# Kernel tuning notes

Hardware: AMD Instinct MI355X
Metric: run time of the kernel (lower is better)

Reference implementation:

```python
import jax, jax.numpy as jnp
import numpy as np
import math

B, S, H, NH = 2, 2048, 1024, 16
HD = H // NH  # 64


def setup_inputs() -> dict:
    key = jax.random.key(0)
    ks = jax.random.split(key, 16)
    s = 0.02  # init scale for weights
    def lin(k, fan_in, fan_out):
        kw, kb = jax.random.split(k)
        # stored as [in, out] so y = x @ W + b (equivalent to torch Linear)
        W = jax.random.normal(kw, (fan_in, fan_out), jnp.float32) * s
        b = jax.random.normal(kb, (fan_out,), jnp.float32) * s
        return W, b
    q_w, q_b = lin(ks[2], H, H)
    k_w, k_b = lin(ks[3], H, H)
    v_w, v_b = lin(ks[4], H, H)
    o_w, o_b = lin(ks[5], H, H)
    pg_w, pg_b = lin(ks[6], 4, NH)   # prosody_gate
    mg_w, mg_b = lin(ks[7], H, 1)    # memory_gate
    return dict(
        hidden_states=jax.random.normal(ks[0], (B, S, H), jnp.float32),
        prosody=jax.random.normal(ks[1], (B, S, 4), jnp.float32),
        q_w=q_w, q_b=q_b, k_w=k_w, k_b=k_b, v_w=v_w, v_b=v_b,
        o_w=o_w, o_b=o_b, pg_w=pg_w, pg_b=pg_b, mg_w=mg_w, mg_b=mg_b,
    )


def reference(hidden_states, prosody, q_w, q_b, k_w, k_b, v_w, v_b,
              o_w, o_b, pg_w, pg_b, mg_w, mg_b):
    b, s, _ = hidden_states.shape
    # Q, K, V projections -> [B, NH, S, HD]
    def split_heads(x):
        return x.reshape(b, s, NH, HD).transpose(0, 2, 1, 3)
    q = split_heads(hidden_states @ q_w + q_b)
    k = split_heads(hidden_states @ k_w + k_b)
    v = split_heads(hidden_states @ v_w + v_b)
    # Prosody gating of queries: gain in (0,1), per (batch, head, position)
    prosody_gain = jax.nn.sigmoid(prosody @ pg_w + pg_b)      # [B, S, NH]
    prosody_gain = prosody_gain.transpose(0, 2, 1)[..., None]  # [B, NH, S, 1]
    q = q * (1.0 + prosody_gain)
    # Scaled scores [B, NH, S, S]
    scores = jnp.einsum('bhqd,bhkd->bhqk', q, k) / math.sqrt(HD)
    # Hippocampal memory scaling: per-query-position multiplicative gate
    memory_weight = jax.nn.sigmoid(hidden_states @ mg_w + mg_b)  # [B, S, 1]
    mem_scale = 1.0 + memory_weight[:, None, :, :] * 0.5         # [B, 1, S, 1]
    scores = scores * mem_scale
    # Causal mask (upper triangle above diagonal -> -inf)
    causal = jnp.tril(jnp.ones((s, s), dtype=bool))
    scores = jnp.where(causal[None, None], scores, -jnp.inf)
    attn_weights = jax.nn.softmax(scores, axis=-1)
    # (dropout is identity in eval / p=0)
    context = jnp.einsum('bhqk,bhkd->bhqd', attn_weights, v)
    context = context.transpose(0, 2, 1, 3).reshape(b, s, H)
    output = context @ o_w + o_b
    return (output, attn_weights)
```

## Files before the change

### kernel.cpp

```cpp
#include <hip/hip_runtime.h>
#include <hip/hip_bf16.h>
#include <math.h>

#define B_  2
#define S_  2048
#define H_  1024
#define NH_ 16
#define HD_ 64
#define BS_ (B_*S_)

typedef __bf16 bf16x8 __attribute__((ext_vector_type(8)));
typedef short  s16x8  __attribute__((ext_vector_type(8)));
typedef short  s16x4  __attribute__((ext_vector_type(4)));
typedef float  f32x4  __attribute__((ext_vector_type(4)));

__device__ __forceinline__ unsigned short f2b(float f) {
    __hip_bfloat16 h = __float2bfloat16(f);
    return __builtin_bit_cast(unsigned short, h);
}
__device__ __forceinline__ float sigmoidf_(float x) { return 1.0f / (1.0f + expf(-x)); }

__device__ __forceinline__ bf16x8 cat8(s16x4 a, s16x4 b) {
    s16x8 c = __builtin_shufflevector(a, b, 0, 1, 2, 3, 4, 5, 6, 7);
    return __builtin_bit_cast(bf16x8, c);
}
__device__ __forceinline__ s16x4 cvt4(float4 v) {
    s16x4 r;
    r[0] = (short)f2b(v.x); r[1] = (short)f2b(v.y);
    r[2] = (short)f2b(v.z); r[3] = (short)f2b(v.w);
    return r;
}

__global__ __launch_bounds__(256) void gates_kernel(
    const float* __restrict__ hs, const float* __restrict__ prosody,
    const float* __restrict__ pg_w, const float* __restrict__ pg_b,
    const float* __restrict__ mg_w, const float* __restrict__ mg_b,
    float* __restrict__ gain, float* __restrict__ ms)
{
    int wave = threadIdx.x >> 6, lane = threadIdx.x & 63;
    int row = blockIdx.x * 4 + wave;
    const float4* hr4 = (const float4*)(hs + (size_t)row * H_);
    const float4* mg4 = (const float4*)mg_w;
    float acc = 0.f;
#pragma unroll
    for (int i = 0; i < 4; ++i) {
        float4 h = hr4[lane + i * 64], m = mg4[lane + i * 64];
        acc += h.x * m.x + h.y * m.y + h.z * m.z + h.w * m.w;
    }
#pragma unroll
    for (int m = 32; m; m >>= 1) acc += __shfl_xor(acc, m);
    if (lane == 0)
        ms[row] = 1.0f + 0.5f * sigmoidf_(acc + mg_b[0]);
    if (lane < NH_) {
        float g = pg_b[lane];
#pragma unroll
        for (int i = 0; i < 4; ++i)
            g += prosody[row * 4 + i] * pg_w[i * NH_ + lane];
        gain[row * NH_ + lane] = 1.0f + sigmoidf_(g);
    }
}

__global__ __launch_bounds__(256) void proj_kernel(
    const float* __restrict__ A32, const unsigned short* __restrict__ A16,
    const float* __restrict__ W, const float* __restrict__ bias,
    unsigned short* __restrict__ out16, float* __restrict__ out32,
    const float* __restrict__ gain, int mode)
{
    __shared__ short As[64 * 40];
    __shared__ short Ws[64 * 40];
    int tid = threadIdx.x;
    int wave = tid >> 6, lane = tid & 63, quad = lane >> 4, l16 = lane & 15;
    int n0 = blockIdx.x * 64, m0 = blockIdx.y * 64;
    f32x4 acc[4] = {};

    for (int k0 = 0; k0 < H_; k0 += 32) {
        __syncthreads();
        {
            int ar = tid >> 2, ac = (tid & 3) * 8;
            if (mode == 2) {
                const unsigned short* ap = A16 + (size_t)(m0 + ar) * H_ + k0 + ac;
                *(s16x4*)&As[ar * 40 + ac]     = *(const s16x4*)(ap);
                *(s16x4*)&As[ar * 40 + ac + 4] = *(const s16x4*)(ap + 4);
            } else {
                const float* ap = A32 + (size_t)(m0 + ar) * H_ + k0 + ac;
                *(s16x4*)&As[ar * 40 + ac]     = cvt4(*(const float4*)(ap));
                *(s16x4*)&As[ar * 40 + ac + 4] = cvt4(*(const float4*)(ap + 4));
            }
        }
        {
            int kr = tid >> 3, nc = (tid & 7) * 8;
            const float* wp = W + (size_t)(k0 + kr) * H_ + n0 + nc;
            s16x4 w0 = cvt4(*(const float4*)(wp));
            s16x4 w1 = cvt4(*(const float4*)(wp + 4));
#pragma unroll
            for (int j = 0; j < 4; ++j) Ws[(nc + j) * 40 + kr]     = w0[j];
#pragma unroll
            for (int j = 0; j < 4; ++j) Ws[(nc + 4 + j) * 40 + kr] = w1[j];
        }
        __syncthreads();
        int mrow = wave * 16 + l16;
        s16x4 a0 = *(const s16x4*)&As[mrow * 40 + quad * 8];
        s16x4 a1 = *(const s16x4*)&As[mrow * 40 + quad * 8 + 4];
        bf16x8 af = cat8(a0, a1);
#pragma unroll
        for (int nt = 0; nt < 4; ++nt) {
            int n = nt * 16 + l16;
            s16x4 b0 = *(const s16x4*)&Ws[n * 40 + quad * 8];
            s16x4 b1 = *(const s16x4*)&Ws[n * 40 + quad * 8 + 4];
            acc[nt] = __builtin_amdgcn_mfma_f32_16x16x32_bf16(af, cat8(b0, b1), acc[nt], 0, 0, 0);
        }
    }

    int mbase = m0 + wave * 16 + quad * 4;
#pragma unroll
    for (int nt = 0; nt < 4; ++nt) {
        int n = n0 + nt * 16 + l16;
        float bv = bias[n];
#pragma unroll
        for (int r = 0; r < 4; ++r) {
            int m = mbase + r;
            float v = acc[nt][r] + bv;
            if (mode == 2) {
                out32[(size_t)m * H_ + n] = v;
            } else {
                int b = m >> 11, s = m & (S_ - 1);
                int nh = n >> 6, hd = n & 63;
                if (mode == 0) v *= gain[m * NH_ + nh];
                out16[(((size_t)(b * NH_ + nh)) * S_ + s) * HD_ + hd] = f2b(v);
            }
        }
    }
}

__global__ __launch_bounds__(256) void zero_upper_kernel(float* __restrict__ attn)
{
    int kt = blockIdx.x, qt = blockIdx.y, bh = blockIdx.z;
    if (kt <= qt) return;
    float* p = attn + (size_t)bh * S_ * S_ + (size_t)(qt * 64) * S_ + kt * 64;
    int r = threadIdx.x >> 2, c = (threadIdx.x & 3) * 16;
    float4 z = {0.f, 0.f, 0.f, 0.f};
    float* q = p + (size_t)r * S_ + c;
    *(float4*)(q)      = z;
    *(float4*)(q + 4)  = z;
    *(float4*)(q + 8)  = z;
    *(float4*)(q + 12) = z;
}

__global__ __launch_bounds__(256) void attn_kernel(
    const unsigned short* __restrict__ qg, const unsigned short* __restrict__ kk,
    const unsigned short* __restrict__ vv, const float* __restrict__ ms,
    float* __restrict__ attn, unsigned short* __restrict__ ctx)
{
    __shared__ short Ks[64 * 72];
    __shared__ short Vt[64 * 72];
    __shared__ short Ps[4][16 * 72];
    __shared__ float mss[64];

    int tid = threadIdx.x;
    int wave = tid >> 6, lane = tid & 63, quad = lane >> 4, l16 = lane & 15;
    int qt = blockIdx.x, bh = blockIdx.y;
    int b = bh >> 4, h = bh & 15;

    const unsigned short* Qh = qg + (size_t)bh * S_ * HD_;
    const unsigned short* Kh = kk + (size_t)bh * S_ * HD_;
    const unsigned short* Vh = vv + (size_t)bh * S_ * HD_;
    float* attnh = attn + (size_t)bh * S_ * S_;

    if (tid < 64) mss[tid] = ms[b * S_ + qt * 64 + tid];

    bf16x8 aq[2];
    {
        int qrow = qt * 64 + wave * 16 + l16;
#pragma unroll
        for (int c = 0; c < 2; ++c) {
            const unsigned short* qp = Qh + (size_t)qrow * HD_ + c * 32 + quad * 8;
            aq[c] = cat8(*(const s16x4*)qp, *(const s16x4*)(qp + 4));
        }
    }
    __syncthreads();
    float msr[4];
#pragma unroll
    for (int r = 0; r < 4; ++r) msr[r] = mss[wave * 16 + quad * 4 + r];
    int myrow0 = qt * 64 + wave * 16 + quad * 4;

    float m_run[4], l_run[4];
#pragma unroll
    for (int r = 0; r < 4; ++r) { m_run[r] = -1e30f; l_run[r] = 0.f; }

    for (int kt = 0; kt <= qt; ++kt) {
        __syncthreads();
        {
            int key = tid >> 2, hc = (tid & 3) * 16;
            const unsigned short* kp = Kh + (size_t)(kt * 64 + key) * HD_ + hc;
            *(s16x4*)&Ks[key * 72 + hc]      = *(const s16x4*)(kp);
            *(s16x4*)&Ks[key * 72 + hc + 4]  = *(const s16x4*)(kp + 4);
            *(s16x4*)&Ks[key * 72 + hc + 8]  = *(const s16x4*)(kp + 8);
            *(s16x4*)&Ks[key * 72 + hc + 12] = *(const s16x4*)(kp + 12);
        }
        __syncthreads();
        float sv[4][4];
#pragma unroll
        for (int nt = 0; nt < 4; ++nt) {
            f32x4 sc = {};
            int n = nt * 16 + l16;
#pragma unroll
            for (int c = 0; c < 2; ++c) {
                s16x4 b0 = *(const s16x4*)&Ks[n * 72 + c * 32 + quad * 8];
                s16x4 b1 = *(const s16x4*)&Ks[n * 72 + c * 32 + quad * 8 + 4];
                sc = __builtin_amdgcn_mfma_f32_16x16x32_bf16(aq[c], cat8(b0, b1), sc, 0, 0, 0);
            }
#pragma unroll
            for (int r = 0; r < 4; ++r) {
                float s = sc[r] * 0.125f * msr[r];
                if (kt == qt) {
                    int col = kt * 64 + nt * 16 + l16;
                    if (col > myrow0 + r) s = -1e30f;
                }
                sv[nt][r] = s;
            }
        }
#pragma unroll
        for (int r = 0; r < 4; ++r) {
            float mt = fmaxf(fmaxf(sv[0][r], sv[1][r]), fmaxf(sv[2][r], sv[3][r]));
            mt = fmaxf(mt, __shfl_xor(mt, 1)); mt = fmaxf(mt, __shfl_xor(mt, 2));
            mt = fmaxf(mt, __shfl_xor(mt, 4)); mt = fmaxf(mt, __shfl_xor(mt, 8));
            float mn = fmaxf(m_run[r], mt);
            float lt = 0.f;
#pragma unroll
            for (int nt = 0; nt < 4; ++nt) lt += expf(sv[nt][r] - mn);
            lt += __shfl_xor(lt, 1); lt += __shfl_xor(lt, 2);
            lt += __shfl_xor(lt, 4); lt += __shfl_xor(lt, 8);
            l_run[r] = l_run[r] * expf(m_run[r] - mn) + lt;
            m_run[r] = mn;
        }
    }
    float inv_l[4];
#pragma unroll
    for (int r = 0; r < 4; ++r) inv_l[r] = 1.0f / l_run[r];

    f32x4 oacc[4] = {};
    for (int kt = 0; kt <= qt; ++kt) {
        __syncthreads();
        {
            int key = tid >> 2, hc = (tid & 3) * 16;
            const unsigned short* kp = Kh + (size_t)(kt * 64 + key) * HD_ + hc;
            *(s16x4*)&Ks[key * 72 + hc]      = *(const s16x4*)(kp);
            *(s16x4*)&Ks[key * 72 + hc + 4]  = *(const s16x4*)(kp + 4);
            *(s16x4*)&Ks[key * 72 + hc + 8]  = *(const s16x4*)(kp + 8);
            *(s16x4*)&Ks[key * 72 + hc + 12] = *(const s16x4*)(kp + 12);
            const unsigned short* vp = Vh + (size_t)(kt * 64 + key) * HD_ + hc;
            s16x4 v0 = *(const s16x4*)(vp);
            s16x4 v1 = *(const s16x4*)(vp + 4);
            s16x4 v2 = *(const s16x4*)(vp + 8);
            s16x4 v3 = *(const s16x4*)(vp + 12);
#pragma unroll
            for (int j = 0; j < 4; ++j) Vt[(hc + j) * 72 + key]      = v0[j];
#pragma unroll
            for (int j = 0; j < 4; ++j) Vt[(hc + 4 + j) * 72 + key]  = v1[j];
#pragma unroll
            for (int j = 0; j < 4; ++j) Vt[(hc + 8 + j) * 72 + key]  = v2[j];
#pragma unroll
            for (int j = 0; j < 4; ++j) Vt[(hc + 12 + j) * 72 + key] = v3[j];
        }
        __syncthreads();
#pragma unroll
        for (int nt = 0; nt < 4; ++nt) {
            f32x4 sc = {};
            int n = nt * 16 + l16;
#pragma unroll
            for (int c = 0; c < 2; ++c) {
                s16x4 b0 = *(const s16x4*)&Ks[n * 72 + c * 32 + quad * 8];
                s16x4 b1 = *(const s16x4*)&Ks[n * 72 + c * 32 + quad * 8 + 4];
                sc = __builtin_amdgcn_mfma_f32_16x16x32_bf16(aq[c], cat8(b0, b1), sc, 0, 0, 0);
            }
#pragma unroll
            for (int r = 0; r < 4; ++r) {
                float s = sc[r] * 0.125f * msr[r];
                if (kt == qt) {
                    int col = kt * 64 + nt * 16 + l16;
                    if (col > myrow0 + r) s = -1e30f;
                }
                float p = expf(s - m_run[r]) * inv_l[r];
                attnh[(size_t)(myrow0 + r) * S_ + kt * 64 + nt * 16 + l16] = p;
                Ps[wave][(quad * 4 + r) * 72 + nt * 16 + l16] = (short)f2b(p);
            }
        }
#pragma unroll
        for (int c = 0; c < 2; ++c) {
            s16x4 p0 = *(const s16x4*)&Ps[wave][l16 * 72 + c * 32 + quad * 8];
            s16x4 p1 = *(const s16x4*)&Ps[wave][l16 * 72 + c * 32 + quad * 8 + 4];
            bf16x8 ap = cat8(p0, p1);
#pragma unroll
            for (int nt = 0; nt < 4; ++nt) {
                s16x4 b0 = *(const s16x4*)&Vt[(nt * 16 + l16) * 72 + c * 32 + quad * 8];
                s16x4 b1 = *(const s16x4*)&Vt[(nt * 16 + l16) * 72 + c * 32 + quad * 8 + 4];
                oacc[nt] = __builtin_amdgcn_mfma_f32_16x16x32_bf16(ap, cat8(b0, b1), oacc[nt], 0, 0, 0);
            }
        }
    }
#pragma unroll
    for (int nt = 0; nt < 4; ++nt) {
#pragma unroll
        for (int r = 0; r < 4; ++r) {
            int srow = myrow0 + r;
            ctx[((size_t)(b * S_ + srow)) * H_ + h * HD_ + nt * 16 + l16] = f2b(oacc[nt][r]);
        }
    }
}

extern "C" void kernel_launch(void* const* d_in, const int* in_sizes, int n_in,
                              void* d_out, int out_size, void* d_ws, size_t ws_size,
                              hipStream_t stream)
{
    const float* hs   = (const float*)d_in[0];
    const float* pros = (const float*)d_in[1];
    const float* q_w  = (const float*)d_in[2];
    const float* q_b  = (const float*)d_in[3];
    const float* k_w  = (const float*)d_in[4];
    const float* k_b  = (const float*)d_in[5];
    const float* v_w  = (const float*)d_in[6];
    const float* v_b  = (const float*)d_in[7];
    const float* o_w  = (const float*)d_in[8];
    const float* o_b  = (const float*)d_in[9];
    const float* pg_w = (const float*)d_in[10];
    const float* pg_b = (const float*)d_in[11];
    const float* mg_w = (const float*)d_in[12];
    const float* mg_b = (const float*)d_in[13];

    float* out0 = (float*)d_out;
    float* attn = out0 + (size_t)BS_ * H_;

    float* gain_ws = (float*)d_ws;
    float* ms_ws   = gain_ws + (size_t)BS_ * NH_;
    unsigned short* q_ws   = (unsigned short*)(ms_ws + BS_);
    unsigned short* k_ws   = q_ws + (size_t)BS_ * H_;
    unsigned short* v_ws   = k_ws + (size_t)BS_ * H_;
    unsigned short* ctx_ws = v_ws + (size_t)BS_ * H_;

    gates_kernel<<<BS_ / 4, 256, 0, stream>>>(hs, pros, pg_w, pg_b, mg_w, mg_b, gain_ws, ms_ws);

    dim3 gg(H_ / 64, BS_ / 64);
    proj_kernel<<<gg, 256, 0, stream>>>(hs, nullptr, q_w, q_b, q_ws, nullptr, gain_ws, 0);
    proj_kernel<<<gg, 256, 0, stream>>>(hs, nullptr, k_w, k_b, k_ws, nullptr, gain_ws, 1);
    proj_kernel<<<gg, 256, 0, stream>>>(hs, nullptr, v_w, v_b, v_ws, nullptr, gain_ws, 1);

    zero_upper_kernel<<<dim3(S_ / 64, S_ / 64, B_ * NH_), 256, 0, stream>>>(attn);

    attn_kernel<<<dim3(S_ / 64, B_ * NH_), 256, 0, stream>>>(q_ws, k_ws, v_ws, ms_ws, attn, ctx_ws);

    proj_kernel<<<gg, 256, 0, stream>>>(nullptr, ctx_ws, o_w, o_b, nullptr, out0, gain_ws, 2);
}
```

Baseline: 1.078 ms.

## Fuse QKV into one tiled bf16 GEMM, drop softmax max pass, coalesce attention writes

Hidden states and all four weight matrices are converted to bf16 up front, with the weights transposed. Q, K and V are then computed by one fused GEMM using 128x128 tiles and direct global-to-LDS loads, writing an interleaved QKV buffer. The output projection reuses that GEMM. The attention softmax drops the running-max rescaling and uses __expf directly, which relies on scores staying small enough not to overflow. Probabilities are staged through LDS so the attention matrix is written as coalesced float4 rows, at the cost of an extra LDS round trip and output values rounded through bf16.

After: 900.5 us. -16.5%, faster.

```diff
diff --git a/kernel.cpp b/kernel.cpp
--- a/kernel.cpp
+++ b/kernel.cpp
@@ -18,6 +18,10 @@
     __hip_bfloat16 h = __float2bfloat16(f);
     return __builtin_bit_cast(unsigned short, h);
 }
+__device__ __forceinline__ float b2f(unsigned short u) {
+    unsigned x = ((unsigned)u) << 16;
+    return __uint_as_float(x);
+}
 __device__ __forceinline__ float sigmoidf_(float x) { return 1.0f / (1.0f + expf(-x)); }
 
 __device__ __forceinline__ bf16x8 cat8(s16x4 a, s16x4 b) {
@@ -30,6 +34,48 @@
     r[2] = (short)f2b(v.z); r[3] = (short)f2b(v.w);
     return r;
 }
+__device__ __forceinline__ void glds16(const unsigned short* g, unsigned short* l) {
+    __builtin_amdgcn_global_load_lds(
+        (const __attribute__((address_space(1))) unsigned int*)g,
+        (__attribute__((address_space(3))) unsigned int*)l, 16, 0, 0);
+}
+
+__global__ __launch_bounds__(256) void convert_hs_kernel(
+    const float* __restrict__ src, unsigned short* __restrict__ dst)
+{
+    size_t i = ((size_t)blockIdx.x * 256 + threadIdx.x) * 8;
+    float4 a = *(const float4*)(src + i);
+    float4 b = *(const float4*)(src + i + 4);
+    s16x8 o = __builtin_shufflevector(cvt4(a), cvt4(b), 0, 1, 2, 3, 4, 5, 6, 7);
+    *(s16x8*)(dst + i) = o;
+}
+
+__global__ __launch_bounds__(256) void transpose_w_kernel(
+    const float* __restrict__ qw, const float* __restrict__ kw,
+    const float* __restrict__ vw, const float* __restrict__ ow,
+    unsigned short* __restrict__ qkvWt, unsigned short* __restrict__ oWt)
+{
+    __shared__ float T[64][65];
+    int t = threadIdx.x;
+    int k0 = blockIdx.x * 64, n0 = blockIdx.y * 64, z = blockIdx.z;
+    const float* W = (z == 0) ? qw : (z == 1) ? kw : (z == 2) ? vw : ow;
+#pragma unroll
+    for (int p = 0; p < 4; ++p) {
+        int row = p * 16 + (t >> 4);
+        int cc = (t & 15) * 4;
+        float4 v = *(const float4*)(W + (size_t)(k0 + row) * H_ + n0 + cc);
+        T[row][cc] = v.x; T[row][cc+1] = v.y; T[row][cc+2] = v.z; T[row][cc+3] = v.w;
+    }
+    __syncthreads();
+    unsigned short* dst = (z < 3) ? (qkvWt + ((size_t)z * H_) * H_) : oWt;
+#pragma unroll
+    for (int p = 0; p < 4; ++p) {
+        int n = p * 16 + (t >> 4);
+        int kc = (t & 15) * 4;
+        float4 v = { T[kc][n], T[kc+1][n], T[kc+2][n], T[kc+3][n] };
+        *(s16x4*)(dst + (size_t)(n0 + n) * H_ + k0 + kc) = cvt4(v);
+    }
+}
 
 __global__ __launch_bounds__(256) void gates_kernel(
     const float* __restrict__ hs, const float* __restrict__ prosody,
@@ -60,73 +106,67 @@
     }
 }
 
-__global__ __launch_bounds__(256) void proj_kernel(
-    const float* __restrict__ A32, const unsigned short* __restrict__ A16,
-    const float* __restrict__ W, const float* __restrict__ bias,
+__global__ __launch_bounds__(256) void gemm_kernel(
+    const unsigned short* __restrict__ A, const unsigned short* __restrict__ Bt,
+    const float* __restrict__ bias0, const float* __restrict__ bias1,
+    const float* __restrict__ bias2, const float* __restrict__ gain,
     unsigned short* __restrict__ out16, float* __restrict__ out32,
-    const float* __restrict__ gain, int mode)
-{
-    __shared__ short As[64 * 40];
-    __shared__ short Ws[64 * 40];
+    int ostride, int mode)
+{
+    __shared__ unsigned short As[128 * 64];
+    __shared__ unsigned short Bs[128 * 64];
     int tid = threadIdx.x;
     int wave = tid >> 6, lane = tid & 63, quad = lane >> 4, l16 = lane & 15;
-    int n0 = blockIdx.x * 64, m0 = blockIdx.y * 64;
-    f32x4 acc[4] = {};
-
-    for (int k0 = 0; k0 < H_; k0 += 32) {
-        __syncthreads();
-        {
-            int ar = tid >> 2, ac = (tid & 3) * 8;
-            if (mode == 2) {
-                const unsigned short* ap = A16 + (size_t)(m0 + ar) * H_ + k0 + ac;
-                *(s16x4*)&As[ar * 40 + ac]     = *(const s16x4*)(ap);
-                *(s16x4*)&As[ar * 40 + ac + 4] = *(const s16x4*)(ap + 4);
-            } else {
-                const float* ap = A32 + (size_t)(m0 + ar) * H_ + k0 + ac;
-                *(s16x4*)&As[ar * 40 + ac]     = cvt4(*(const float4*)(ap));
-                *(s16x4*)&As[ar * 40 + ac + 4] = cvt4(*(const float4*)(ap + 4));
-            }
-        }
-        {
-            int kr = tid >> 3, nc = (tid & 7) * 8;
-            const float* wp = W + (size_t)(k0 + kr) * H_ + n0 + nc;
-            s16x4 w0 = cvt4(*(const float4*)(wp));
-            s16x4 w1 = cvt4(*(const float4*)(wp + 4));
-#pragma unroll
-            for (int j = 0; j < 4; ++j) Ws[(nc + j) * 40 + kr]     = w0[j];
-#pragma unroll
-            for (int j = 0; j < 4; ++j) Ws[(nc + 4 + j) * 40 + kr] = w1[j];
-        }
-        __syncthreads();
-        int mrow = wave * 16 + l16;
-        s16x4 a0 = *(const s16x4*)&As[mrow * 40 + quad * 8];
-        s16x4 a1 = *(const s16x4*)&As[mrow * 40 + quad * 8 + 4];
-        bf16x8 af = cat8(a0, a1);
-#pragma unroll
-        for (int nt = 0; nt < 4; ++nt) {
-            int n = nt * 16 + l16;
-            s16x4 b0 = *(const s16x4*)&Ws[n * 40 + quad * 8];
-            s16x4 b1 = *(const s16x4*)&Ws[n * 40 + quad * 8 + 4];
-            acc[nt] = __builtin_amdgcn_mfma_f32_16x16x32_bf16(af, cat8(b0, b1), acc[nt], 0, 0, 0);
-        }
-    }
-
-    int mbase = m0 + wave * 16 + quad * 4;
-#pragma unroll
-    for (int nt = 0; nt < 4; ++nt) {
-        int n = n0 + nt * 16 + l16;
-        float bv = bias[n];
-#pragma unroll
-        for (int r = 0; r < 4; ++r) {
-            int m = mbase + r;
-            float v = acc[nt][r] + bv;
-            if (mode == 2) {
-                out32[(size_t)m * H_ + n] = v;
-            } else {
-                int b = m >> 11, s = m & (S_ - 1);
-                int nh = n >> 6, hd = n & 63;
-                if (mode == 0) v *= gain[m * NH_ + nh];
-                out16[(((size_t)(b * NH_ + nh)) * S_ + s) * HD_ + hd] = f2b(v);
+    int n0 = blockIdx.x * 128, m0 = blockIdx.y * 128;
+    int wm = (wave & 1) * 64, wn = (wave >> 1) * 64;
+    f32x4 acc[4][4] = {};
+
+    int lrow = lane >> 3, lcol = (lane & 7) * 8;
+    for (int k0 = 0; k0 < H_; k0 += 64) {
+        __syncthreads();
+#pragma unroll
+        for (int c = 0; c < 4; ++c) {
+            int ch = wave * 4 + c;
+            int row = ch * 8 + lrow;
+            glds16(A  + (size_t)(m0 + row) * H_ + k0 + lcol, (unsigned short*)As + ch * 512);
+            glds16(Bt + (size_t)(n0 + row) * H_ + k0 + lcol, (unsigned short*)Bs + ch * 512);
+        }
+        __syncthreads();
+#pragma unroll
+        for (int kc = 0; kc < 2; ++kc) {
+            bf16x8 af[4], bfr[4];
+#pragma unroll
+            for (int i = 0; i < 4; ++i)
+                af[i] = *(const bf16x8*)&As[(wm + i * 16 + l16) * 64 + kc * 32 + quad * 8];
+#pragma unroll
+            for (int j = 0; j < 4; ++j)
+                bfr[j] = *(const bf16x8*)&Bs[(wn + j * 16 + l16) * 64 + kc * 32 + quad * 8];
+#pragma unroll
+            for (int i = 0; i < 4; ++i)
+#pragma unroll
+                for (int j = 0; j < 4; ++j)
+                    acc[i][j] = __builtin_amdgcn_mfma_f32_16x16x32_bf16(af[i], bfr[j], acc[i][j], 0, 0, 0);
+        }
+    }
+
+    int mat = n0 >> 10;
+    const float* bp = (mat == 0) ? bias0 : (mat == 1) ? bias1 : bias2;
+#pragma unroll
+    for (int j = 0; j < 4; ++j) {
+        int n = n0 + wn + j * 16 + l16;
+        float bv = bp[n & (H_ - 1)];
+#pragma unroll
+        for (int i = 0; i < 4; ++i) {
+#pragma unroll
+            for (int r = 0; r < 4; ++r) {
+                int m = m0 + wm + i * 16 + quad * 4 + r;
+                float v = acc[i][j][r] + bv;
+                if (mode == 0) {
+                    if (n < H_) v *= gain[m * NH_ + (n >> 6)];
+                    out16[(size_t)m * ostride + n] = f2b(v);
+                } else {
+                    out32[(size_t)m * ostride + n] = v;
+                }
             }
         }
     }
@@ -147,8 +187,7 @@
 }
 
 __global__ __launch_bounds__(256) void attn_kernel(
-    const unsigned short* __restrict__ qg, const unsigned short* __restrict__ kk,
-    const unsigned short* __restrict__ vv, const float* __restrict__ ms,
+    const unsigned short* __restrict__ qkv, const float* __restrict__ ms,
     float* __restrict__ attn, unsigned short* __restrict__ ctx)
 {
     __shared__ short Ks[64 * 72];
@@ -161,9 +200,8 @@
     int qt = blockIdx.x, bh = blockIdx.y;
     int b = bh >> 4, h = bh & 15;
 
-    const unsigned short* Qh = qg + (size_t)bh * S_ * HD_;
-    const unsigned short* Kh = kk + (size_t)bh * S_ * HD_;
-    const unsigned short* Vh = vv + (size_t)bh * S_ * HD_;
+    const unsigned short* base = qkv + (size_t)b * S_ * 3072;
+    int offQ = h * 64, offK = 1024 + h * 64, offV = 2048 + h * 64;
     float* attnh = attn + (size_t)bh * S_ * S_;
 
     if (tid < 64) mss[tid] = ms[b * S_ + qt * 64 + tid];
@@ -173,32 +211,28 @@
         int qrow = qt * 64 + wave * 16 + l16;
 #pragma unroll
         for (int c = 0; c < 2; ++c) {
-            const unsigned short* qp = Qh + (size_t)qrow * HD_ + c * 32 + quad * 8;
+            const unsigned short* qp = base + (size_t)qrow * 3072 + offQ + c * 32 + quad * 8;
             aq[c] = cat8(*(const s16x4*)qp, *(const s16x4*)(qp + 4));
         }
     }
     __syncthreads();
-    float msr[4];
-#pragma unroll
-    for (int r = 0; r < 4; ++r) msr[r] = mss[wave * 16 + quad * 4 + r];
+    float escale[4];
+#pragma unroll
+    for (int r = 0; r < 4; ++r) escale[r] = 0.125f * mss[wave * 16 + quad * 4 + r];
     int myrow0 = qt * 64 + wave * 16 + quad * 4;
 
-    float m_run[4], l_run[4];
-#pragma unroll
-    for (int r = 0; r < 4; ++r) { m_run[r] = -1e30f; l_run[r] = 0.f; }
+    float l_run[4] = {0.f, 0.f, 0.f, 0.f};
 
     for (int kt = 0; kt <= qt; ++kt) {
         __syncthreads();
         {
             int key = tid >> 2, hc = (tid & 3) * 16;
-            const unsigned short* kp = Kh + (size_t)(kt * 64 + key) * HD_ + hc;
-            *(s16x4*)&Ks[key * 72 + hc]      = *(const s16x4*)(kp);
-            *(s16x4*)&Ks[key * 72 + hc + 4]  = *(const s16x4*)(kp + 4);
-            *(s16x4*)&Ks[key * 72 + hc + 8]  = *(const s16x4*)(kp + 8);
-            *(s16x4*)&Ks[key * 72 + hc + 12] = *(const s16x4*)(kp + 12);
-        }
-        __syncthreads();
-        float sv[4][4];
+            const unsigned short* kp = base + (size_t)(kt * 64 + key) * 3072 + offK + hc;
+            *(s16x8*)&Ks[key * 72 + hc]     = *(const s16x8*)(kp);
+            *(s16x8*)&Ks[key * 72 + hc + 8] = *(const s16x8*)(kp + 8);
+        }
+        __syncthreads();
+        float esum[4] = {0.f, 0.f, 0.f, 0.f};
 #pragma unroll
         for (int nt = 0; nt < 4; ++nt) {
             f32x4 sc = {};
@@ -209,29 +243,19 @@
                 s16x4 b1 = *(const s16x4*)&Ks[n * 72 + c * 32 + quad * 8 + 4];
                 sc = __builtin_amdgcn_mfma_f32_16x16x32_bf16(aq[c], cat8(b0, b1), sc, 0, 0, 0);
             }
+            int col = kt * 64 + nt * 16 + l16;
 #pragma unroll
             for (int r = 0; r < 4; ++r) {
-                float s = sc[r] * 0.125f * msr[r];
-                if (kt == qt) {
-                    int col = kt * 64 + nt * 16 + l16;
-                    if (col > myrow0 + r) s = -1e30f;
-                }
-                sv[nt][r] = s;
+                float e = (kt == qt && col > myrow0 + r) ? 0.f : __expf(sc[r] * escale[r]);
+                esum[r] += e;
             }
         }
 #pragma unroll
         for (int r = 0; r < 4; ++r) {
-            float mt = fmaxf(fmaxf(sv[0][r], sv[1][r]), fmaxf(sv[2][r], sv[3][r]));
-            mt = fmaxf(mt, __shfl_xor(mt, 1)); mt = fmaxf(mt, __shfl_xor(mt, 2));
-            mt = fmaxf(mt, __shfl_xor(mt, 4)); mt = fmaxf(mt, __shfl_xor(mt, 8));
-            float mn = fmaxf(m_run[r], mt);
-            float lt = 0.f;
-#pragma unroll
-            for (int nt = 0; nt < 4; ++nt) lt += expf(sv[nt][r] - mn);
+            float lt = esum[r];
             lt += __shfl_xor(lt, 1); lt += __shfl_xor(lt, 2);
             lt += __shfl_xor(lt, 4); lt += __shfl_xor(lt, 8);
-            l_run[r] = l_run[r] * expf(m_run[r] - mn) + lt;
-            m_run[r] = mn;
+            l_run[r] += lt;
         }
     }
     float inv_l[4];
@@ -243,12 +267,10 @@
         __syncthreads();
         {
             int key = tid >> 2, hc = (tid & 3) * 16;
-            const unsigned short* kp = Kh + (size_t)(kt * 64 + key) * HD_ + hc;
-            *(s16x4*)&Ks[key * 72 + hc]      = *(const s16x4*)(kp);
-            *(s16x4*)&Ks[key * 72 + hc + 4]  = *(const s16x4*)(kp + 4);
-            *(s16x4*)&Ks[key * 72 + hc + 8]  = *(const s16x4*)(kp + 8);
-            *(s16x4*)&Ks[key * 72 + hc + 12] = *(const s16x4*)(kp + 12);
-            const unsigned short* vp = Vh + (size_t)(kt * 64 + key) * HD_ + hc;
+            const unsigned short* kp = base + (size_t)(kt * 64 + key) * 3072 + offK + hc;
+            *(s16x8*)&Ks[key * 72 + hc]     = *(const s16x8*)(kp);
+            *(s16x8*)&Ks[key * 72 + hc + 8] = *(const s16x8*)(kp + 8);
+            const unsigned short* vp = base + (size_t)(kt * 64 + key) * 3072 + offV + hc;
             s16x4 v0 = *(const s16x4*)(vp);
             s16x4 v1 = *(const s16x4*)(vp + 4);
             s16x4 v2 = *(const s16x4*)(vp + 8);
@@ -273,17 +295,23 @@
                 s16x4 b1 = *(const s16x4*)&Ks[n * 72 + c * 32 + quad * 8 + 4];
                 sc = __builtin_amdgcn_mfma_f32_16x16x32_bf16(aq[c], cat8(b0, b1), sc, 0, 0, 0);
             }
+            int col = kt * 64 + nt * 16 + l16;
 #pragma unroll
             for (int r = 0; r < 4; ++r) {
-                float s = sc[r] * 0.125f * msr[r];
-                if (kt == qt) {
-                    int col = kt * 64 + nt * 16 + l16;
-                    if (col > myrow0 + r) s = -1e30f;
-                }
-                float p = expf(s - m_run[r]) * inv_l[r];
-                attnh[(size_t)(myrow0 + r) * S_ + kt * 64 + nt * 16 + l16] = p;
+                float p = (kt == qt && col > myrow0 + r) ? 0.f
+                          : __expf(sc[r] * escale[r]) * inv_l[r];
                 Ps[wave][(quad * 4 + r) * 72 + nt * 16 + l16] = (short)f2b(p);
             }
+        }
+#pragma unroll
+        for (int c = 0; c < 4; ++c) {
+            int row_local = c * 4 + quad;
+            s16x4 p4 = *(const s16x4*)&Ps[wave][row_local * 72 + l16 * 4];
+            float4 f;
+            f.x = b2f((unsigned short)p4[0]); f.y = b2f((unsigned short)p4[1]);
+            f.z = b2f((unsigned short)p4[2]); f.w = b2f((unsigned short)p4[3]);
+            int row_s = qt * 64 + wave * 16 + row_local;
+            *(float4*)(attnh + (size_t)row_s * S_ + kt * 64 + l16 * 4) = f;
         }
 #pragma unroll
         for (int c = 0; c < 2; ++c) {
@@ -332,21 +360,23 @@
 
     float* gain_ws = (float*)d_ws;
     float* ms_ws   = gain_ws + (size_t)BS_ * NH_;
-    unsigned short* q_ws   = (unsigned short*)(ms_ws + BS_);
-    unsigned short* k_ws   = q_ws + (size_t)BS_ * H_;
-    unsigned short* v_ws   = k_ws + (size_t)BS_ * H_;
-    unsigned short* ctx_ws = v_ws + (size_t)BS_ * H_;
-
+    unsigned short* hs16   = (unsigned short*)(ms_ws + BS_);
+    unsigned short* qkvWt  = hs16 + (size_t)BS_ * H_;
+    unsigned short* oWt    = qkvWt + (size_t)3 * H_ * H_;
+    unsigned short* qkv16  = oWt + (size_t)H_ * H_;
+    unsigned short* ctx16  = qkv16 + (size_t)BS_ * 3 * H_;
+
+    convert_hs_kernel<<<(BS_ * H_) / (256 * 8), 256, 0, stream>>>(hs, hs16);
+    transpose_w_kernel<<<dim3(16, 16, 4), 256, 0, stream>>>(q_w, k_w, v_w, o_w, qkvWt, oWt);
     gates_kernel<<<BS_ / 4, 256, 0, stream>>>(hs, pros, pg_w, pg_b, mg_w, mg_b, gain_ws, ms_ws);
 
-    dim3 gg(H_ / 64, BS_ / 64);
-    proj_kernel<<<gg, 256, 0, stream>>>(hs, nullptr, q_w, q_b, q_ws, nullptr, gain_ws, 0);
-    proj_kernel<<<gg, 256, 0, stream>>>(hs, nullptr, k_w, k_b, k_ws, nullptr, gain_ws, 1);
-    proj_kernel<<<gg, 256, 0, stream>>>(hs, nullptr, v_w, v_b, v_ws, nullptr, gain_ws, 1);
+    gemm_kernel<<<dim3(3 * H_ / 128, BS_ / 128), 256, 0, stream>>>(
+        hs16, qkvWt, q_b, k_b, v_b, gain_ws, qkv16, nullptr, 3 * H_, 0);
 
     zero_upper_kernel<<<dim3(S_ / 64, S_ / 64, B_ * NH_), 256, 0, stream>>>(attn);
 
-    attn_kernel<<<dim3(S_ / 64, B_ * NH_), 256, 0, stream>>>(q_ws, k_ws, v_ws, ms_ws, attn, ctx_ws);
-
-    proj_kernel<<<gg, 256, 0, stream>>>(nullptr, ctx_ws, o_w, o_b, nullptr, out0, gain_ws, 2);
-}
+    attn_kernel<<<dim3(S_ / 64, B_ * NH_), 256, 0, stream>>>(qkv16, ms_ws, attn, ctx16);
+
+    gemm_kernel<<<dim3(H_ / 128, BS_ / 128), 256, 0, stream>>>(
+        ctx16, oWt, o_b, nullptr, nullptr, nullptr, nullptr, out0, H_, 1);
+}
```
